# Performance work log

Hardware: AMD Instinct MI355X
Metric: run time of the kernel (lower is better)

## Reference

```python
import jax, jax.numpy as jnp
import numpy as np

B, S, D_MODEL = 1, 4096, 2048
N_HEADS, N_KV_HEADS, HEAD_DIM = 16, 4, 128
N_KV_GROUPS = N_HEADS // N_KV_HEADS  # 4


def rotate_half(x):
    h = x.shape[-1] // 2
    return jnp.concatenate([-x[..., h:], x[..., :h]], axis=-1)


def setup_inputs() -> dict:
    key = jax.random.key(0)
    k1, k2, k3, k4, k5 = jax.random.split(key, 5)
    hidden_states = jax.random.normal(k1, (B, S, D_MODEL), dtype=jnp.float32)
    # RoPE tables: [S, HEAD_DIM]
    inv_freq = 1.0 / (10000.0 ** (jnp.arange(0, HEAD_DIM, 2, dtype=jnp.float32) / HEAD_DIM))
    t = jnp.arange(S, dtype=jnp.float32)
    freqs = jnp.outer(t, inv_freq)                      # [S, HEAD_DIM/2]
    emb = jnp.concatenate([freqs, freqs], axis=-1)      # [S, HEAD_DIM]
    cos, sin = jnp.cos(emb), jnp.sin(emb)
    scale = 0.02
    Wq = jax.random.normal(k2, (D_MODEL, N_HEADS * HEAD_DIM), dtype=jnp.float32) * scale
    Wk = jax.random.normal(k3, (D_MODEL, N_KV_HEADS * HEAD_DIM), dtype=jnp.float32) * scale
    Wv = jax.random.normal(k4, (D_MODEL, N_KV_HEADS * HEAD_DIM), dtype=jnp.float32) * scale
    Wo = jax.random.normal(k5, (N_HEADS * HEAD_DIM, D_MODEL), dtype=jnp.float32) * scale
    return {"hidden_states": hidden_states, "cos": cos, "sin": sin,
            "Wq": Wq, "Wk": Wk, "Wv": Wv, "Wo": Wo}


def reference(hidden_states, cos, sin, Wq, Wk, Wv, Wo):
    b, s, _ = hidden_states.shape
    # projections -> [b, heads, s, head_dim]
    q = (hidden_states @ Wq).reshape(b, s, N_HEADS, HEAD_DIM).transpose(0, 2, 1, 3)
    k = (hidden_states @ Wk).reshape(b, s, N_KV_HEADS, HEAD_DIM).transpose(0, 2, 1, 3)
    v = (hidden_states @ Wv).reshape(b, s, N_KV_HEADS, HEAD_DIM).transpose(0, 2, 1, 3)
    # RoPE (cos/sin broadcast over batch and heads)
    c = cos[None, None, :, :]
    si = sin[None, None, :, :]
    q = q * c + rotate_half(q) * si
    k = k * c + rotate_half(k) * si
    # expand KV heads to match query heads (GQA)
    k = jnp.repeat(k, N_KV_GROUPS, axis=1)  # [b, N_HEADS, s, d]
    v = jnp.repeat(v, N_KV_GROUPS, axis=1)
    # attention scores with causal mask
    scores = jnp.einsum('bhqd,bhkd->bhqk', q, k) / jnp.sqrt(jnp.float32(HEAD_DIM))
    causal = jnp.tril(jnp.ones((s, s), dtype=bool))
    scores = jnp.where(causal[None, None], scores, jnp.float32(-jnp.inf))
    probs = jax.nn.softmax(scores.astype(jnp.float32), axis=-1).astype(q.dtype)
    out = jnp.einsum('bhqk,bhkd->bhqd', probs, v)
    out = out.transpose(0, 2, 1, 3).reshape(b, s, N_HEADS * HEAD_DIM)
    return out @ Wo
```

## Files before the change

### kernel.cpp

```cpp
#include <hip/hip_runtime.h>
#include <hip/hip_bf16.h>

#define S_LEN 4096
#define DMODEL 2048
#define NH 16
#define NKV 4
#define HD 128

typedef __bf16 bf16x8 __attribute__((ext_vector_type(8)));
typedef float f32x4 __attribute__((ext_vector_type(4)));
typedef unsigned short u16x8 __attribute__((ext_vector_type(8)));
typedef unsigned short u16x4 __attribute__((ext_vector_type(4)));
typedef unsigned long long u64x2 __attribute__((ext_vector_type(2)));

__device__ __forceinline__ unsigned short f2bf(float f) {
    unsigned int u = __builtin_bit_cast(unsigned int, f);
    u += 0x7fffu + ((u >> 16) & 1u);
    return (unsigned short)(u >> 16);
}
__device__ __forceinline__ float bf2f(unsigned short h) {
    unsigned int u = ((unsigned int)h) << 16;
    return __builtin_bit_cast(float, u);
}

__device__ __forceinline__ unsigned int cvt_pk_bf16(float lo, float hi) {
    unsigned int r;
    asm("v_cvt_pk_bf16_f32 %0, %1, %2" : "=v"(r) : "v"(lo), "v"(hi));
    return r;
}

__device__ __forceinline__ float fast_exp2(float x) {
    float r;
    asm("v_exp_f32 %0, %1" : "=v"(r) : "v"(x));
    return r;
}

__device__ __forceinline__ f32x4 mfma16(bf16x8 a, bf16x8 b, f32x4 c) {
    return __builtin_amdgcn_mfma_f32_16x16x32_bf16(a, b, c, 0, 0, 0);
}

__device__ __forceinline__ void async16(unsigned short* lds, const unsigned short* g) {
    __builtin_amdgcn_global_load_lds((__attribute__((address_space(1))) void*)g,
                                     (__attribute__((address_space(3))) void*)lds,
                                     16, 0, 0);
}

__global__ __launch_bounds__(256) void conv_f32_bf16(
    const float* __restrict__ in, unsigned short* __restrict__ out, int n4) {
    int i = blockIdx.x * 256 + threadIdx.x;
    if (i >= n4) return;
    float4 v = *(const float4*)&in[(size_t)i * 4];
    u16x4 o;
    o[0] = f2bf(v.x); o[1] = f2bf(v.y); o[2] = f2bf(v.z); o[3] = f2bf(v.w);
    *(u16x4*)&out[(size_t)i * 4] = o;
}

__global__ __launch_bounds__(1024) void transpose_f32_bf16(
    const float* __restrict__ in, unsigned short* __restrict__ out,
    int R, int C) {
    __shared__ float tile[32][33];
    int x = blockIdx.x * 32 + threadIdx.x;
    int y = blockIdx.y * 32 + threadIdx.y;
    tile[threadIdx.y][threadIdx.x] = in[(size_t)y * C + x];
    __syncthreads();
    int ox = blockIdx.y * 32 + threadIdx.x;
    int oy = blockIdx.x * 32 + threadIdx.y;
    out[(size_t)oy * R + ox] = f2bf(tile[threadIdx.x][threadIdx.y]);
}

__global__ __launch_bounds__(1024) void transpose_bf16(
    const unsigned short* __restrict__ in, unsigned short* __restrict__ out,
    int R, int C, int ldin) {
    __shared__ unsigned short tile[32][33];
    int x = blockIdx.x * 32 + threadIdx.x;
    int y = blockIdx.y * 32 + threadIdx.y;
    tile[threadIdx.y][threadIdx.x] = in[(size_t)y * ldin + x];
    __syncthreads();
    int ox = blockIdx.y * 32 + threadIdx.x;
    int oy = blockIdx.x * 32 + threadIdx.y;
    out[(size_t)oy * R + ox] = tile[threadIdx.x][threadIdx.y];
}

template <typename OutT>
__global__ __launch_bounds__(256) void gemm_bt(
    const unsigned short* __restrict__ A, const unsigned short* __restrict__ Bt,
    OutT* __restrict__ C, int N, int K) {
    __shared__ __align__(16) unsigned short As[2][128 * 32];
    __shared__ __align__(16) unsigned short Bs[2][128 * 32];
    const int tid = threadIdx.x;
    const int wave = tid >> 6, lane = tid & 63, quad = lane >> 4, l16 = lane & 15;
    const int m0 = blockIdx.x * 128, n0 = blockIdx.y * 128;
    const int waveM = (wave & 1) * 64, waveN = (wave >> 1) * 64;
    f32x4 acc[4][4] = {};

    auto stage = [&](int k0, int b) {
#pragma unroll
        for (int u = 0; u < 2; u++) {
            const int seg = wave * 2 + u;
            const int idx = seg * 64 + lane;
            const int r = idx >> 2, c = idx & 3;
            async16(&As[b][seg * 512], &A[(size_t)(m0 + r) * K + k0 + c * 8]);
            async16(&Bs[b][seg * 512], &Bt[(size_t)(n0 + r) * K + k0 + c * 8]);
        }
    };

    const int niter = K / 32;
    stage(0, 0);
    __syncthreads();
    for (int it = 0; it < niter; it++) {
        const int b = it & 1;
        if (it + 1 < niter) stage((it + 1) * 32, b ^ 1);
        bf16x8 af[4], bfv[4];
#pragma unroll
        for (int i = 0; i < 4; i++)
            af[i] = *(const bf16x8*)&As[b][(waveM + i * 16 + l16) * 32 + quad * 8];
#pragma unroll
        for (int j = 0; j < 4; j++)
            bfv[j] = *(const bf16x8*)&Bs[b][(waveN + j * 16 + l16) * 32 + quad * 8];
#pragma unroll
        for (int i = 0; i < 4; i++)
#pragma unroll
            for (int j = 0; j < 4; j++)
                acc[i][j] = mfma16(af[i], bfv[j], acc[i][j]);
        __syncthreads();
    }
#pragma unroll
    for (int i = 0; i < 4; i++)
#pragma unroll
        for (int j = 0; j < 4; j++)
#pragma unroll
            for (int r = 0; r < 4; r++) {
                int row = m0 + waveM + i * 16 + quad * 4 + r;
                int col = n0 + waveN + j * 16 + l16;
                if constexpr (sizeof(OutT) == 2)
                    C[(size_t)row * N + col] = f2bf(acc[i][j][r]);
                else
                    C[(size_t)row * N + col] = acc[i][j][r];
            }
}

__global__ __launch_bounds__(256) void rope_kernel(
    unsigned short* __restrict__ X, const float* __restrict__ cb,
    const float* __restrict__ sb, int log2nh, int stride) {
    int idx = blockIdx.x * 256 + threadIdx.x;
    int d = idx & 63;
    int h = (idx >> 6) & ((1 << log2nh) - 1);
    int s = idx >> (6 + log2nh);
    size_t base = (size_t)s * stride + h * HD + d;
    float a = bf2f(X[base]);
    float b = bf2f(X[base + 64]);
    float c0 = cb[s * HD + d];
    float s0 = sb[s * HD + d];
    float c1 = cb[s * HD + d + 64];
    float s1 = sb[s * HD + d + 64];
    X[base]      = f2bf(a * c0 - b * s0);
    X[base + 64] = f2bf(b * c1 + a * s1);
}

__global__ __launch_bounds__(256, 2) void attn_kernel(
    const unsigned short* __restrict__ Q, const unsigned short* __restrict__ Kv,
    const unsigned short* __restrict__ Vt, unsigned short* __restrict__ O) {
    __shared__ __align__(16) unsigned short Kt[2][64 * 128];
    __shared__ __align__(16) unsigned short Vs[2][128 * 64];
    __shared__ __align__(16) unsigned long long Ps[4 * 4 * 64];
    const int tid = threadIdx.x;
    const int wave = tid >> 6, lane = tid & 63, quad = lane >> 4, l16 = lane & 15;
    const int id = blockIdx.x;
    const int h = id & 15;
    const int qb = (id < 256) ? (31 - (id >> 4)) : ((id - 256) >> 4);
    const int kvh = h >> 2;
    const int rowbase = qb * 128 + wave * 32;
    unsigned long long* Pw = &Ps[wave * 4 * 64];
    const float cexp = 0.08838834764831845f * 1.44269504088896f;

    auto stage = [&](int c, int b) {
        const int kb = c * 64;
#pragma unroll
        for (int u = 0; u < 4; u++) {
            const int seg = wave * 4 + u;
            const int idx = seg * 64 + lane;
            {
                const int r = idx >> 4, cs = idx & 15, cl = cs ^ (r & 15);
                async16(&Kt[b][seg * 512],
                        &Kv[(size_t)(kb + r) * (NKV * HD * 2) + kvh * HD + cl * 8]);
            }
            {
                const int r = idx >> 3, cs = idx & 7, cl = cs ^ (r & 7);
                async16(&Vs[b][seg * 512],
                        &Vt[(size_t)(kvh * HD + r) * S_LEN + kb + cl * 8]);
            }
        }
    };

    bf16x8 qf[2][4];
#pragma unroll
    for (int i = 0; i < 2; i++)
#pragma unroll
        for (int dd = 0; dd < 4; dd++)
            qf[i][dd] = *(const bf16x8*)&Q[(size_t)(rowbase + i * 16 + l16) * DMODEL +
                                           h * HD + dd * 32 + quad * 8];

    f32x4 oacc[2][8] = {};
    float lrow[2] = {0.0f, 0.0f};
    const int qa0 = rowbase + l16;
    const int qa1 = rowbase + 16 + l16;
    const int nch = 2 * (qb + 1);

    stage(0, 0);
    __syncthreads();
    for (int c = 0; c < nch; c++) {
        const int b = c & 1;
        if (c + 1 < nch) stage(c + 1, b ^ 1);
        const int kb = c * 64;
        if (kb <= rowbase + 31) {
            const bool diag = (kb + 63 > rowbase);
#pragma unroll
            for (int kk = 0; kk < 2; kk++) {
                f32x4 sacc[2][2] = {};
                __builtin_amdgcn_s_setprio(1);
#pragma unroll
                for (int dd = 0; dd < 4; dd++) {
                    const int csw = (dd * 4 + quad) ^ l16;
                    bf16x8 kf0 = *(const bf16x8*)&Kt[b][(((2 * kk + 0) * 16 + l16) * 16 + csw) * 8];
                    bf16x8 kf1 = *(const bf16x8*)&Kt[b][(((2 * kk + 1) * 16 + l16) * 16 + csw) * 8];
                    sacc[0][0] = mfma16(kf0, qf[0][dd], sacc[0][0]);
                    sacc[0][1] = mfma16(kf1, qf[0][dd], sacc[0][1]);
                    sacc[1][0] = mfma16(kf0, qf[1][dd], sacc[1][0]);
                    sacc[1][1] = mfma16(kf1, qf[1][dd], sacc[1][1]);
                }
                __builtin_amdgcn_s_setprio(0);
#pragma unroll
                for (int i = 0; i < 2; i++) {
                    const int qa = i ? qa1 : qa0;
#pragma unroll
                    for (int jl = 0; jl < 2; jl++) {
                        const int kg = kb + 16 * (2 * kk + jl) + 4 * quad;
                        float p0 = fast_exp2(sacc[i][jl][0] * cexp);
                        float p1 = fast_exp2(sacc[i][jl][1] * cexp);
                        float p2 = fast_exp2(sacc[i][jl][2] * cexp);
                        float p3 = fast_exp2(sacc[i][jl][3] * cexp);
                        if (diag) {
                            if (kg + 0 > qa) p0 = 0.0f;
                            if (kg + 1 > qa) p1 = 0.0f;
                            if (kg + 2 > qa) p2 = 0.0f;
                            if (kg + 3 > qa) p3 = 0.0f;
                        }
                        lrow[i] += (p0 + p1) + (p2 + p3);
                        unsigned int lo = cvt_pk_bf16(p0, p1);
                        unsigned int hi = cvt_pk_bf16(p2, p3);
                        Pw[(i * 2 + jl) * 64 + lane] =
                            (unsigned long long)lo | ((unsigned long long)hi << 32);
                    }
                }
                bf16x8 pf[2];
#pragma unroll
                for (int i = 0; i < 2; i++) {
                    const unsigned long long* src =
                        &Pw[(i * 2 + (quad >> 1)) * 64 + l16 + 32 * (quad & 1)];
                    u64x2 t;
                    t[0] = src[0];
                    t[1] = src[16];
                    pf[i] = __builtin_bit_cast(bf16x8, t);
                }
                const int vsw0 = ((kk * 4 + quad) ^ (l16 & 7)) * 8;
                __builtin_amdgcn_s_setprio(1);
#pragma unroll
                for (int jd = 0; jd < 8; jd++) {
                    bf16x8 vf = *(const bf16x8*)&Vs[b][(jd * 16 + l16) * 64 + vsw0];
                    oacc[0][jd] = mfma16(pf[0], vf, oacc[0][jd]);
                    oacc[1][jd] = mfma16(pf[1], vf, oacc[1][jd]);
                }
                __builtin_amdgcn_s_setprio(0);
            }
        }
        __syncthreads();
    }
    float lsum[2];
#pragma unroll
    for (int i = 0; i < 2; i++) {
        float l = lrow[i];
        l += __shfl_xor(l, 16, 64);
        l += __shfl_xor(l, 32, 64);
        lsum[i] = l;
    }
#pragma unroll
    for (int i = 0; i < 2; i++)
#pragma unroll
        for (int r = 0; r < 4; r++) {
            float lq = __shfl(lsum[i], quad * 4 + r, 64);
            float inv = 1.0f / lq;
            int row = rowbase + i * 16 + quad * 4 + r;
#pragma unroll
            for (int jd = 0; jd < 8; jd++)
                O[(size_t)row * DMODEL + h * HD + jd * 16 + l16] = f2bf(oacc[i][jd][r] * inv);
        }
}

extern "C" void kernel_launch(void* const* d_in, const int* in_sizes, int n_in,
                              void* d_out, int out_size, void* d_ws, size_t ws_size,
                              hipStream_t stream) {
    const float* X  = (const float*)d_in[0];
    const float* cb = (const float*)d_in[1];
    const float* sb = (const float*)d_in[2];
    const float* Wq = (const float*)d_in[3];
    const float* Wk = (const float*)d_in[4];
    const float* Wv = (const float*)d_in[5];
    const float* Wo = (const float*)d_in[6];
    float* out = (float*)d_out;

    char* ws = (char*)d_ws;
    size_t off = 0;
    auto alloc = [&](size_t bytes) { char* p = ws + off; off += (bytes + 255) & ~(size_t)255; return p; };
    unsigned short* Xb   = (unsigned short*)alloc((size_t)S_LEN * DMODEL * 2);
    unsigned short* Qb   = (unsigned short*)alloc((size_t)S_LEN * DMODEL * 2);
    unsigned short* KVb  = (unsigned short*)alloc((size_t)S_LEN * 2 * NKV * HD * 2);
    unsigned short* Vtb  = (unsigned short*)alloc((size_t)S_LEN * NKV * HD * 2);
    unsigned short* Ob   = (unsigned short*)alloc((size_t)S_LEN * DMODEL * 2);
    unsigned short* WqT  = (unsigned short*)alloc((size_t)DMODEL * DMODEL * 2);
    unsigned short* WkvT = (unsigned short*)alloc((size_t)DMODEL * 2 * NKV * HD * 2);
    unsigned short* WoT  = (unsigned short*)alloc((size_t)DMODEL * DMODEL * 2);

    conv_f32_bf16<<<(S_LEN * DMODEL / 4 + 255) / 256, 256, 0, stream>>>(X, Xb, S_LEN * DMODEL / 4);

    dim3 tb(32, 32);
    transpose_f32_bf16<<<dim3(DMODEL / 32, DMODEL / 32), tb, 0, stream>>>(Wq, WqT, DMODEL, DMODEL);
    transpose_f32_bf16<<<dim3((NKV * HD) / 32, DMODEL / 32), tb, 0, stream>>>(Wk, WkvT, DMODEL, NKV * HD);
    transpose_f32_bf16<<<dim3((NKV * HD) / 32, DMODEL / 32), tb, 0, stream>>>(Wv, WkvT + (size_t)(NKV * HD) * DMODEL, DMODEL, NKV * HD);
    transpose_f32_bf16<<<dim3(DMODEL / 32, DMODEL / 32), tb, 0, stream>>>(Wo, WoT, DMODEL, DMODEL);

    gemm_bt<unsigned short><<<dim3(S_LEN / 128, DMODEL / 128), 256, 0, stream>>>(Xb, WqT, Qb, DMODEL, DMODEL);
    gemm_bt<unsigned short><<<dim3(S_LEN / 128, (2 * NKV * HD) / 128), 256, 0, stream>>>(Xb, WkvT, KVb, 2 * NKV * HD, DMODEL);

    rope_kernel<<<(S_LEN * NH * 64) / 256, 256, 0, stream>>>(Qb, cb, sb, 4, DMODEL);
    rope_kernel<<<(S_LEN * NKV * 64) / 256, 256, 0, stream>>>(KVb, cb, sb, 2, 2 * NKV * HD);

    transpose_bf16<<<dim3((NKV * HD) / 32, S_LEN / 32), tb, 0, stream>>>(
        KVb + NKV * HD, Vtb, S_LEN, NKV * HD, 2 * NKV * HD);

    attn_kernel<<<512, 256, 0, stream>>>(Qb, KVb, Vtb, Ob);

    gemm_bt<float><<<dim3(S_LEN / 128, DMODEL / 128), 256, 0, stream>>>(Ob, WoT, out, DMODEL, DMODEL);
}
```

Before: 420.4 us.

## Fuse QKV projection GEMM and halve attention tile to 64 query rows

Concatenates Wq, Wk and Wv into one transposed weight so a single GEMM produces Q, K and V in one interleaved buffer, replacing the two separate projection launches. The attention kernel is retiled from 128 query rows per block (32 per wave) to 64 (16 per wave), with 32-key chunks, smaller shared buffers, a new query-block ordering across 1024 blocks, and launch bounds raised to 4 blocks per CU. The smaller tiles aim for higher occupancy and better causal load balance, at the cost of less K/V reuse per load and more loop iterations and barriers.

After: 382.9 us. -8.9%, faster.

```diff
diff --git a/kernel.cpp b/kernel.cpp
--- a/kernel.cpp
+++ b/kernel.cpp
@@ -6,6 +6,7 @@
 #define NH 16
 #define NKV 4
 #define HD 128
+#define QKV_N 3072
 
 typedef __bf16 bf16x8 __attribute__((ext_vector_type(8)));
 typedef float f32x4 __attribute__((ext_vector_type(4)));
@@ -157,143 +158,128 @@
     X[base + 64] = f2bf(b * c1 + a * s1);
 }
 
-__global__ __launch_bounds__(256, 2) void attn_kernel(
+__global__ __launch_bounds__(256, 4) void attn_kernel(
     const unsigned short* __restrict__ Q, const unsigned short* __restrict__ Kv,
     const unsigned short* __restrict__ Vt, unsigned short* __restrict__ O) {
-    __shared__ __align__(16) unsigned short Kt[2][64 * 128];
-    __shared__ __align__(16) unsigned short Vs[2][128 * 64];
-    __shared__ __align__(16) unsigned long long Ps[4 * 4 * 64];
+    __shared__ __align__(16) unsigned short Kt[2][32 * 128];
+    __shared__ __align__(16) unsigned short Vs[2][128 * 32];
+    __shared__ __align__(16) unsigned long long Ps[4 * 2 * 64];
     const int tid = threadIdx.x;
     const int wave = tid >> 6, lane = tid & 63, quad = lane >> 4, l16 = lane & 15;
     const int id = blockIdx.x;
     const int h = id & 15;
-    const int qb = (id < 256) ? (31 - (id >> 4)) : ((id - 256) >> 4);
+    const int grp = id >> 4, g = grp & 15, quarter = grp >> 4;
+    const int qb = quarter == 0 ? 63 - g : quarter == 1 ? g
+                 : quarter == 2 ? 32 + g : 31 - g;
     const int kvh = h >> 2;
-    const int rowbase = qb * 128 + wave * 32;
-    unsigned long long* Pw = &Ps[wave * 4 * 64];
+    const int rowbase = qb * 64 + wave * 16;
+    unsigned long long* Pw = &Ps[wave * 2 * 64];
     const float cexp = 0.08838834764831845f * 1.44269504088896f;
 
     auto stage = [&](int c, int b) {
-        const int kb = c * 64;
-#pragma unroll
-        for (int u = 0; u < 4; u++) {
-            const int seg = wave * 4 + u;
+        const int kb = c * 32;
+#pragma unroll
+        for (int u = 0; u < 2; u++) {
+            const int seg = wave * 2 + u;
             const int idx = seg * 64 + lane;
             {
                 const int r = idx >> 4, cs = idx & 15, cl = cs ^ (r & 15);
                 async16(&Kt[b][seg * 512],
-                        &Kv[(size_t)(kb + r) * (NKV * HD * 2) + kvh * HD + cl * 8]);
+                        &Kv[(size_t)(kb + r) * QKV_N + kvh * HD + cl * 8]);
             }
             {
-                const int r = idx >> 3, cs = idx & 7, cl = cs ^ (r & 7);
+                const int r = idx >> 2, cs = idx & 3, cl = cs ^ ((r >> 1) & 3);
                 async16(&Vs[b][seg * 512],
                         &Vt[(size_t)(kvh * HD + r) * S_LEN + kb + cl * 8]);
             }
         }
     };
 
-    bf16x8 qf[2][4];
-#pragma unroll
-    for (int i = 0; i < 2; i++)
-#pragma unroll
-        for (int dd = 0; dd < 4; dd++)
-            qf[i][dd] = *(const bf16x8*)&Q[(size_t)(rowbase + i * 16 + l16) * DMODEL +
-                                           h * HD + dd * 32 + quad * 8];
-
-    f32x4 oacc[2][8] = {};
-    float lrow[2] = {0.0f, 0.0f};
-    const int qa0 = rowbase + l16;
-    const int qa1 = rowbase + 16 + l16;
-    const int nch = 2 * (qb + 1);
+    bf16x8 qf[4];
+#pragma unroll
+    for (int dd = 0; dd < 4; dd++)
+        qf[dd] = *(const bf16x8*)&Q[(size_t)(rowbase + l16) * QKV_N +
+                                     h * HD + dd * 32 + quad * 8];
+
+    f32x4 oacc[8] = {};
+    float lrow = 0.0f;
+    const int qa = rowbase + l16;
+    const int nch = 2 * qb + 2;
 
     stage(0, 0);
     __syncthreads();
     for (int c = 0; c < nch; c++) {
         const int b = c & 1;
         if (c + 1 < nch) stage(c + 1, b ^ 1);
-        const int kb = c * 64;
-        if (kb <= rowbase + 31) {
-            const bool diag = (kb + 63 > rowbase);
-#pragma unroll
-            for (int kk = 0; kk < 2; kk++) {
-                f32x4 sacc[2][2] = {};
-                __builtin_amdgcn_s_setprio(1);
-#pragma unroll
-                for (int dd = 0; dd < 4; dd++) {
-                    const int csw = (dd * 4 + quad) ^ l16;
-                    bf16x8 kf0 = *(const bf16x8*)&Kt[b][(((2 * kk + 0) * 16 + l16) * 16 + csw) * 8];
-                    bf16x8 kf1 = *(const bf16x8*)&Kt[b][(((2 * kk + 1) * 16 + l16) * 16 + csw) * 8];
-                    sacc[0][0] = mfma16(kf0, qf[0][dd], sacc[0][0]);
-                    sacc[0][1] = mfma16(kf1, qf[0][dd], sacc[0][1]);
-                    sacc[1][0] = mfma16(kf0, qf[1][dd], sacc[1][0]);
-                    sacc[1][1] = mfma16(kf1, qf[1][dd], sacc[1][1]);
+        const int kb = c * 32;
+        if (kb <= rowbase + 15) {
+            const bool diag = (kb + 31 > rowbase);
+            f32x4 sacc[2] = {};
+            __builtin_amdgcn_s_setprio(1);
+#pragma unroll
+            for (int dd = 0; dd < 4; dd++) {
+                const int csw = (dd * 4 + quad) ^ l16;
+                bf16x8 kf0 = *(const bf16x8*)&Kt[b][((0 * 16 + l16) * 16 + csw) * 8];
+                bf16x8 kf1 = *(const bf16x8*)&Kt[b][((1 * 16 + l16) * 16 + csw) * 8];
+                sacc[0] = mfma16(kf0, qf[dd], sacc[0]);
+                sacc[1] = mfma16(kf1, qf[dd], sacc[1]);
+            }
+            __builtin_amdgcn_s_setprio(0);
+#pragma unroll
+            for (int jl = 0; jl < 2; jl++) {
+                const int kg = kb + 16 * jl + 4 * quad;
+                float p0 = fast_exp2(sacc[jl][0] * cexp);
+                float p1 = fast_exp2(sacc[jl][1] * cexp);
+                float p2 = fast_exp2(sacc[jl][2] * cexp);
+                float p3 = fast_exp2(sacc[jl][3] * cexp);
+                if (diag) {
+                    if (kg + 0 > qa) p0 = 0.0f;
+                    if (kg + 1 > qa) p1 = 0.0f;
+                    if (kg + 2 > qa) p2 = 0.0f;
+                    if (kg + 3 > qa) p3 = 0.0f;
                 }
-                __builtin_amdgcn_s_setprio(0);
-#pragma unroll
-                for (int i = 0; i < 2; i++) {
-                    const int qa = i ? qa1 : qa0;
-#pragma unroll
-                    for (int jl = 0; jl < 2; jl++) {
-                        const int kg = kb + 16 * (2 * kk + jl) + 4 * quad;
-                        float p0 = fast_exp2(sacc[i][jl][0] * cexp);
-                        float p1 = fast_exp2(sacc[i][jl][1] * cexp);
-                        float p2 = fast_exp2(sacc[i][jl][2] * cexp);
-                        float p3 = fast_exp2(sacc[i][jl][3] * cexp);
-                        if (diag) {
-                            if (kg + 0 > qa) p0 = 0.0f;
-                            if (kg + 1 > qa) p1 = 0.0f;
-                            if (kg + 2 > qa) p2 = 0.0f;
-                            if (kg + 3 > qa) p3 = 0.0f;
-                        }
-                        lrow[i] += (p0 + p1) + (p2 + p3);
-                        unsigned int lo = cvt_pk_bf16(p0, p1);
-                        unsigned int hi = cvt_pk_bf16(p2, p3);
-                        Pw[(i * 2 + jl) * 64 + lane] =
-                            (unsigned long long)lo | ((unsigned long long)hi << 32);
-                    }
-                }
-                bf16x8 pf[2];
-#pragma unroll
-                for (int i = 0; i < 2; i++) {
-                    const unsigned long long* src =
-                        &Pw[(i * 2 + (quad >> 1)) * 64 + l16 + 32 * (quad & 1)];
-                    u64x2 t;
-                    t[0] = src[0];
-                    t[1] = src[16];
-                    pf[i] = __builtin_bit_cast(bf16x8, t);
-                }
-                const int vsw0 = ((kk * 4 + quad) ^ (l16 & 7)) * 8;
-                __builtin_amdgcn_s_setprio(1);
-#pragma unroll
-                for (int jd = 0; jd < 8; jd++) {
-                    bf16x8 vf = *(const bf16x8*)&Vs[b][(jd * 16 + l16) * 64 + vsw0];
-                    oacc[0][jd] = mfma16(pf[0], vf, oacc[0][jd]);
-                    oacc[1][jd] = mfma16(pf[1], vf, oacc[1][jd]);
-                }
-                __builtin_amdgcn_s_setprio(0);
-            }
+                lrow += (p0 + p1) + (p2 + p3);
+                unsigned int lo = cvt_pk_bf16(p0, p1);
+                unsigned int hi = cvt_pk_bf16(p2, p3);
+                Pw[jl * 64 + lane] =
+                    (unsigned long long)lo | ((unsigned long long)hi << 32);
+            }
+            bf16x8 pf;
+            {
+                const unsigned long long* src =
+                    &Pw[(quad >> 1) * 64 + l16 + 32 * (quad & 1)];
+                u64x2 t;
+                t[0] = src[0];
+                t[1] = src[16];
+                pf = __builtin_bit_cast(bf16x8, t);
+            }
+            const int vsw0 = (quad ^ ((l16 >> 1) & 3)) * 8;
+            __builtin_amdgcn_s_setprio(1);
+#pragma unroll
+            for (int jd = 0; jd < 8; jd++) {
+                bf16x8 vf = *(const bf16x8*)&Vs[b][(jd * 16 + l16) * 32 + vsw0];
+                oacc[jd] = mfma16(pf, vf, oacc[jd]);
+            }
+            __builtin_amdgcn_s_setprio(0);
         }
         __syncthreads();
     }
-    float lsum[2];
-#pragma unroll
-    for (int i = 0; i < 2; i++) {
-        float l = lrow[i];
+    float lsum;
+    {
+        float l = lrow;
         l += __shfl_xor(l, 16, 64);
         l += __shfl_xor(l, 32, 64);
-        lsum[i] = l;
+        lsum = l;
     }
 #pragma unroll
-    for (int i = 0; i < 2; i++)
-#pragma unroll
-        for (int r = 0; r < 4; r++) {
-            float lq = __shfl(lsum[i], quad * 4 + r, 64);
-            float inv = 1.0f / lq;
-            int row = rowbase + i * 16 + quad * 4 + r;
-#pragma unroll
-            for (int jd = 0; jd < 8; jd++)
-                O[(size_t)row * DMODEL + h * HD + jd * 16 + l16] = f2bf(oacc[i][jd][r] * inv);
-        }
+    for (int r = 0; r < 4; r++) {
+        float lq = __shfl(lsum, quad * 4 + r, 64);
+        float inv = 1.0f / lq;
+        int row = rowbase + quad * 4 + r;
+#pragma unroll
+        for (int jd = 0; jd < 8; jd++)
+            O[(size_t)row * DMODEL + h * HD + jd * 16 + l16] = f2bf(oacc[jd][r] * inv);
+    }
 }
 
 extern "C" void kernel_launch(void* const* d_in, const int* in_sizes, int n_in,
@@ -311,33 +297,30 @@
     char* ws = (char*)d_ws;
     size_t off = 0;
     auto alloc = [&](size_t bytes) { char* p = ws + off; off += (bytes + 255) & ~(size_t)255; return p; };
-    unsigned short* Xb   = (unsigned short*)alloc((size_t)S_LEN * DMODEL * 2);
-    unsigned short* Qb   = (unsigned short*)alloc((size_t)S_LEN * DMODEL * 2);
-    unsigned short* KVb  = (unsigned short*)alloc((size_t)S_LEN * 2 * NKV * HD * 2);
-    unsigned short* Vtb  = (unsigned short*)alloc((size_t)S_LEN * NKV * HD * 2);
-    unsigned short* Ob   = (unsigned short*)alloc((size_t)S_LEN * DMODEL * 2);
-    unsigned short* WqT  = (unsigned short*)alloc((size_t)DMODEL * DMODEL * 2);
-    unsigned short* WkvT = (unsigned short*)alloc((size_t)DMODEL * 2 * NKV * HD * 2);
-    unsigned short* WoT  = (unsigned short*)alloc((size_t)DMODEL * DMODEL * 2);
+    unsigned short* Xb    = (unsigned short*)alloc((size_t)S_LEN * DMODEL * 2);
+    unsigned short* QKVb  = (unsigned short*)alloc((size_t)S_LEN * QKV_N * 2);
+    unsigned short* Vtb   = (unsigned short*)alloc((size_t)S_LEN * NKV * HD * 2);
+    unsigned short* Ob    = (unsigned short*)alloc((size_t)S_LEN * DMODEL * 2);
+    unsigned short* WqkvT = (unsigned short*)alloc((size_t)QKV_N * DMODEL * 2);
+    unsigned short* WoT   = (unsigned short*)alloc((size_t)DMODEL * DMODEL * 2);
 
     conv_f32_bf16<<<(S_LEN * DMODEL / 4 + 255) / 256, 256, 0, stream>>>(X, Xb, S_LEN * DMODEL / 4);
 
     dim3 tb(32, 32);
-    transpose_f32_bf16<<<dim3(DMODEL / 32, DMODEL / 32), tb, 0, stream>>>(Wq, WqT, DMODEL, DMODEL);
-    transpose_f32_bf16<<<dim3((NKV * HD) / 32, DMODEL / 32), tb, 0, stream>>>(Wk, WkvT, DMODEL, NKV * HD);
-    transpose_f32_bf16<<<dim3((NKV * HD) / 32, DMODEL / 32), tb, 0, stream>>>(Wv, WkvT + (size_t)(NKV * HD) * DMODEL, DMODEL, NKV * HD);
+    transpose_f32_bf16<<<dim3(DMODEL / 32, DMODEL / 32), tb, 0, stream>>>(Wq, WqkvT, DMODEL, DMODEL);
+    transpose_f32_bf16<<<dim3((NKV * HD) / 32, DMODEL / 32), tb, 0, stream>>>(Wk, WqkvT + (size_t)DMODEL * DMODEL, DMODEL, NKV * HD);
+    transpose_f32_bf16<<<dim3((NKV * HD) / 32, DMODEL / 32), tb, 0, stream>>>(Wv, WqkvT + (size_t)(DMODEL + NKV * HD) * DMODEL, DMODEL, NKV * HD);
     transpose_f32_bf16<<<dim3(DMODEL / 32, DMODEL / 32), tb, 0, stream>>>(Wo, WoT, DMODEL, DMODEL);
 
-    gemm_bt<unsigned short><<<dim3(S_LEN / 128, DMODEL / 128), 256, 0, stream>>>(Xb, WqT, Qb, DMODEL, DMODEL);
-    gemm_bt<unsigned short><<<dim3(S_LEN / 128, (2 * NKV * HD) / 128), 256, 0, stream>>>(Xb, WkvT, KVb, 2 * NKV * HD, DMODEL);
-
-    rope_kernel<<<(S_LEN * NH * 64) / 256, 256, 0, stream>>>(Qb, cb, sb, 4, DMODEL);
-    rope_kernel<<<(S_LEN * NKV * 64) / 256, 256, 0, stream>>>(KVb, cb, sb, 2, 2 * NKV * HD);
+    gemm_bt<unsigned short><<<dim3(S_LEN / 128, QKV_N / 128), 256, 0, stream>>>(Xb, WqkvT, QKVb, QKV_N, DMODEL);
+
+    rope_kernel<<<(S_LEN * NH * 64) / 256, 256, 0, stream>>>(QKVb, cb, sb, 4, QKV_N);
+    rope_kernel<<<(S_LEN * NKV * 64) / 256, 256, 0, stream>>>(QKVb + DMODEL, cb, sb, 2, QKV_N);
 
     transpose_bf16<<<dim3((NKV * HD) / 32, S_LEN / 32), tb, 0, stream>>>(
-        KVb + NKV * HD, Vtb, S_LEN, NKV * HD, 2 * NKV * HD);
-
-    attn_kernel<<<512, 256, 0, stream>>>(Qb, KVb, Vtb, Ob);
+        QKVb + DMODEL + NKV * HD, Vtb, S_LEN, NKV * HD, QKV_N);
+
+    attn_kernel<<<1024, 256, 0, stream>>>(QKVb, QKVb + DMODEL, Vtb, Ob);
 
     gemm_bt<float><<<dim3(S_LEN / 128, DMODEL / 128), 256, 0, stream>>>(Ob, WoT, out, DMODEL, DMODEL);
 }
```

## Fuse Q and KV projections into one GEMM and halve attention KV tile

Applied to the files above, without the earlier changes.

The Q, K and V projections are merged into a single GEMM over a concatenated transposed weight, producing one interleaved QKV buffer. This removes a separate launch and fills the grid better. The attention kernel now stages 32-key chunks instead of 64, halving shared memory per block and raising the launch-bounds occupancy target from 2 to 4 blocks. The cost is twice as many barrier-synchronised iterations, each doing less MFMA work.

Measured after the change: 595.1 us. +41.6%, slower.

```diff
diff --git a/kernel.cpp b/kernel.cpp
--- a/kernel.cpp
+++ b/kernel.cpp
@@ -6,6 +6,7 @@
 #define NH 16
 #define NKV 4
 #define HD 128
+#define QKV_N 3072
 
 typedef __bf16 bf16x8 __attribute__((ext_vector_type(8)));
 typedef float f32x4 __attribute__((ext_vector_type(4)));
@@ -157,11 +158,11 @@
     X[base + 64] = f2bf(b * c1 + a * s1);
 }
 
-__global__ __launch_bounds__(256, 2) void attn_kernel(
+__global__ __launch_bounds__(256, 4) void attn_kernel(
     const unsigned short* __restrict__ Q, const unsigned short* __restrict__ Kv,
     const unsigned short* __restrict__ Vt, unsigned short* __restrict__ O) {
-    __shared__ __align__(16) unsigned short Kt[2][64 * 128];
-    __shared__ __align__(16) unsigned short Vs[2][128 * 64];
+    __shared__ __align__(16) unsigned short Kt[2][32 * 128];
+    __shared__ __align__(16) unsigned short Vs[2][128 * 32];
     __shared__ __align__(16) unsigned long long Ps[4 * 4 * 64];
     const int tid = threadIdx.x;
     const int wave = tid >> 6, lane = tid & 63, quad = lane >> 4, l16 = lane & 15;
@@ -174,18 +175,18 @@
     const float cexp = 0.08838834764831845f * 1.44269504088896f;
 
     auto stage = [&](int c, int b) {
-        const int kb = c * 64;
-#pragma unroll
-        for (int u = 0; u < 4; u++) {
-            const int seg = wave * 4 + u;
+        const int kb = c * 32;
+#pragma unroll
+        for (int u = 0; u < 2; u++) {
+            const int seg = wave * 2 + u;
             const int idx = seg * 64 + lane;
             {
                 const int r = idx >> 4, cs = idx & 15, cl = cs ^ (r & 15);
                 async16(&Kt[b][seg * 512],
-                        &Kv[(size_t)(kb + r) * (NKV * HD * 2) + kvh * HD + cl * 8]);
+                        &Kv[(size_t)(kb + r) * QKV_N + kvh * HD + cl * 8]);
             }
             {
-                const int r = idx >> 3, cs = idx & 7, cl = cs ^ (r & 7);
+                const int r = idx >> 2, cs = idx & 3, cl = cs ^ ((r >> 1) & 3);
                 async16(&Vs[b][seg * 512],
                         &Vt[(size_t)(kvh * HD + r) * S_LEN + kb + cl * 8]);
             }
@@ -197,81 +198,78 @@
     for (int i = 0; i < 2; i++)
 #pragma unroll
         for (int dd = 0; dd < 4; dd++)
-            qf[i][dd] = *(const bf16x8*)&Q[(size_t)(rowbase + i * 16 + l16) * DMODEL +
+            qf[i][dd] = *(const bf16x8*)&Q[(size_t)(rowbase + i * 16 + l16) * QKV_N +
                                            h * HD + dd * 32 + quad * 8];
 
     f32x4 oacc[2][8] = {};
     float lrow[2] = {0.0f, 0.0f};
     const int qa0 = rowbase + l16;
     const int qa1 = rowbase + 16 + l16;
-    const int nch = 2 * (qb + 1);
+    const int nch = 4 * qb + 4;
 
     stage(0, 0);
     __syncthreads();
     for (int c = 0; c < nch; c++) {
         const int b = c & 1;
         if (c + 1 < nch) stage(c + 1, b ^ 1);
-        const int kb = c * 64;
+        const int kb = c * 32;
         if (kb <= rowbase + 31) {
-            const bool diag = (kb + 63 > rowbase);
-#pragma unroll
-            for (int kk = 0; kk < 2; kk++) {
-                f32x4 sacc[2][2] = {};
-                __builtin_amdgcn_s_setprio(1);
-#pragma unroll
-                for (int dd = 0; dd < 4; dd++) {
-                    const int csw = (dd * 4 + quad) ^ l16;
-                    bf16x8 kf0 = *(const bf16x8*)&Kt[b][(((2 * kk + 0) * 16 + l16) * 16 + csw) * 8];
-                    bf16x8 kf1 = *(const bf16x8*)&Kt[b][(((2 * kk + 1) * 16 + l16) * 16 + csw) * 8];
-                    sacc[0][0] = mfma16(kf0, qf[0][dd], sacc[0][0]);
-                    sacc[0][1] = mfma16(kf1, qf[0][dd], sacc[0][1]);
-                    sacc[1][0] = mfma16(kf0, qf[1][dd], sacc[1][0]);
-                    sacc[1][1] = mfma16(kf1, qf[1][dd], sacc[1][1]);
+            const bool diag = (kb + 31 > rowbase);
+            f32x4 sacc[2][2] = {};
+            __builtin_amdgcn_s_setprio(1);
+#pragma unroll
+            for (int dd = 0; dd < 4; dd++) {
+                const int csw = (dd * 4 + quad) ^ l16;
+                bf16x8 kf0 = *(const bf16x8*)&Kt[b][((0 * 16 + l16) * 16 + csw) * 8];
+                bf16x8 kf1 = *(const bf16x8*)&Kt[b][((1 * 16 + l16) * 16 + csw) * 8];
+                sacc[0][0] = mfma16(kf0, qf[0][dd], sacc[0][0]);
+                sacc[0][1] = mfma16(kf1, qf[0][dd], sacc[0][1]);
+                sacc[1][0] = mfma16(kf0, qf[1][dd], sacc[1][0]);
+                sacc[1][1] = mfma16(kf1, qf[1][dd], sacc[1][1]);
+            }
+            __builtin_amdgcn_s_setprio(0);
+#pragma unroll
+            for (int i = 0; i < 2; i++) {
+                const int qa = i ? qa1 : qa0;
+#pragma unroll
+                for (int jl = 0; jl < 2; jl++) {
+                    const int kg = kb + 16 * jl + 4 * quad;
+                    float p0 = fast_exp2(sacc[i][jl][0] * cexp);
+                    float p1 = fast_exp2(sacc[i][jl][1] * cexp);
+                    float p2 = fast_exp2(sacc[i][jl][2] * cexp);
+                    float p3 = fast_exp2(sacc[i][jl][3] * cexp);
+                    if (diag) {
+                        if (kg + 0 > qa) p0 = 0.0f;
+                        if (kg + 1 > qa) p1 = 0.0f;
+                        if (kg + 2 > qa) p2 = 0.0f;
+                        if (kg + 3 > qa) p3 = 0.0f;
+                    }
+                    lrow[i] += (p0 + p1) + (p2 + p3);
+                    unsigned int lo = cvt_pk_bf16(p0, p1);
+                    unsigned int hi = cvt_pk_bf16(p2, p3);
+                    Pw[(i * 2 + jl) * 64 + lane] =
+                        (unsigned long long)lo | ((unsigned long long)hi << 32);
                 }
-                __builtin_amdgcn_s_setprio(0);
-#pragma unroll
-                for (int i = 0; i < 2; i++) {
-                    const int qa = i ? qa1 : qa0;
-#pragma unroll
-                    for (int jl = 0; jl < 2; jl++) {
-                        const int kg = kb + 16 * (2 * kk + jl) + 4 * quad;
-                        float p0 = fast_exp2(sacc[i][jl][0] * cexp);
-                        float p1 = fast_exp2(sacc[i][jl][1] * cexp);
-                        float p2 = fast_exp2(sacc[i][jl][2] * cexp);
-                        float p3 = fast_exp2(sacc[i][jl][3] * cexp);
-                        if (diag) {
-                            if (kg + 0 > qa) p0 = 0.0f;
-                            if (kg + 1 > qa) p1 = 0.0f;
-                            if (kg + 2 > qa) p2 = 0.0f;
-                            if (kg + 3 > qa) p3 = 0.0f;
-                        }
-                        lrow[i] += (p0 + p1) + (p2 + p3);
-                        unsigned int lo = cvt_pk_bf16(p0, p1);
-                        unsigned int hi = cvt_pk_bf16(p2, p3);
-                        Pw[(i * 2 + jl) * 64 + lane] =
-                            (unsigned long long)lo | ((unsigned long long)hi << 32);
-                    }
-                }
-                bf16x8 pf[2];
-#pragma unroll
-                for (int i = 0; i < 2; i++) {
-                    const unsigned long long* src =
-                        &Pw[(i * 2 + (quad >> 1)) * 64 + l16 + 32 * (quad & 1)];
-                    u64x2 t;
-                    t[0] = src[0];
-                    t[1] = src[16];
-                    pf[i] = __builtin_bit_cast(bf16x8, t);
-                }
-                const int vsw0 = ((kk * 4 + quad) ^ (l16 & 7)) * 8;
-                __builtin_amdgcn_s_setprio(1);
-#pragma unroll
-                for (int jd = 0; jd < 8; jd++) {
-                    bf16x8 vf = *(const bf16x8*)&Vs[b][(jd * 16 + l16) * 64 + vsw0];
-                    oacc[0][jd] = mfma16(pf[0], vf, oacc[0][jd]);
-                    oacc[1][jd] = mfma16(pf[1], vf, oacc[1][jd]);
-                }
-                __builtin_amdgcn_s_setprio(0);
-            }
+            }
+            bf16x8 pf[2];
+#pragma unroll
+            for (int i = 0; i < 2; i++) {
+                const unsigned long long* src =
+                    &Pw[(i * 2 + (quad >> 1)) * 64 + l16 + 32 * (quad & 1)];
+                u64x2 t;
+                t[0] = src[0];
+                t[1] = src[16];
+                pf[i] = __builtin_bit_cast(bf16x8, t);
+            }
+            const int vsw0 = (quad ^ ((l16 >> 1) & 3)) * 8;
+            __builtin_amdgcn_s_setprio(1);
+#pragma unroll
+            for (int jd = 0; jd < 8; jd++) {
+                bf16x8 vf = *(const bf16x8*)&Vs[b][(jd * 16 + l16) * 32 + vsw0];
+                oacc[0][jd] = mfma16(pf[0], vf, oacc[0][jd]);
+                oacc[1][jd] = mfma16(pf[1], vf, oacc[1][jd]);
+            }
+            __builtin_amdgcn_s_setprio(0);
         }
         __syncthreads();
     }
@@ -311,33 +309,30 @@
     char* ws = (char*)d_ws;
     size_t off = 0;
     auto alloc = [&](size_t bytes) { char* p = ws + off; off += (bytes + 255) & ~(size_t)255; return p; };
-    unsigned short* Xb   = (unsigned short*)alloc((size_t)S_LEN * DMODEL * 2);
-    unsigned short* Qb   = (unsigned short*)alloc((size_t)S_LEN * DMODEL * 2);
-    unsigned short* KVb  = (unsigned short*)alloc((size_t)S_LEN * 2 * NKV * HD * 2);
-    unsigned short* Vtb  = (unsigned short*)alloc((size_t)S_LEN * NKV * HD * 2);
-    unsigned short* Ob   = (unsigned short*)alloc((size_t)S_LEN * DMODEL * 2);
-    unsigned short* WqT  = (unsigned short*)alloc((size_t)DMODEL * DMODEL * 2);
-    unsigned short* WkvT = (unsigned short*)alloc((size_t)DMODEL * 2 * NKV * HD * 2);
-    unsigned short* WoT  = (unsigned short*)alloc((size_t)DMODEL * DMODEL * 2);
+    unsigned short* Xb    = (unsigned short*)alloc((size_t)S_LEN * DMODEL * 2);
+    unsigned short* QKVb  = (unsigned short*)alloc((size_t)S_LEN * QKV_N * 2);
+    unsigned short* Vtb   = (unsigned short*)alloc((size_t)S_LEN * NKV * HD * 2);
+    unsigned short* Ob    = (unsigned short*)alloc((size_t)S_LEN * DMODEL * 2);
+    unsigned short* WqkvT = (unsigned short*)alloc((size_t)QKV_N * DMODEL * 2);
+    unsigned short* WoT   = (unsigned short*)alloc((size_t)DMODEL * DMODEL * 2);
 
     conv_f32_bf16<<<(S_LEN * DMODEL / 4 + 255) / 256, 256, 0, stream>>>(X, Xb, S_LEN * DMODEL / 4);
 
     dim3 tb(32, 32);
-    transpose_f32_bf16<<<dim3(DMODEL / 32, DMODEL / 32), tb, 0, stream>>>(Wq, WqT, DMODEL, DMODEL);
-    transpose_f32_bf16<<<dim3((NKV * HD) / 32, DMODEL / 32), tb, 0, stream>>>(Wk, WkvT, DMODEL, NKV * HD);
-    transpose_f32_bf16<<<dim3((NKV * HD) / 32, DMODEL / 32), tb, 0, stream>>>(Wv, WkvT + (size_t)(NKV * HD) * DMODEL, DMODEL, NKV * HD);
+    transpose_f32_bf16<<<dim3(DMODEL / 32, DMODEL / 32), tb, 0, stream>>>(Wq, WqkvT, DMODEL, DMODEL);
+    transpose_f32_bf16<<<dim3((NKV * HD) / 32, DMODEL / 32), tb, 0, stream>>>(Wk, WqkvT + (size_t)DMODEL * DMODEL, DMODEL, NKV * HD);
+    transpose_f32_bf16<<<dim3((NKV * HD) / 32, DMODEL / 32), tb, 0, stream>>>(Wv, WqkvT + (size_t)(DMODEL + NKV * HD) * DMODEL, DMODEL, NKV * HD);
     transpose_f32_bf16<<<dim3(DMODEL / 32, DMODEL / 32), tb, 0, stream>>>(Wo, WoT, DMODEL, DMODEL);
 
-    gemm_bt<unsigned short><<<dim3(S_LEN / 128, DMODEL / 128), 256, 0, stream>>>(Xb, WqT, Qb, DMODEL, DMODEL);
-    gemm_bt<unsigned short><<<dim3(S_LEN / 128, (2 * NKV * HD) / 128), 256, 0, stream>>>(Xb, WkvT, KVb, 2 * NKV * HD, DMODEL);
-
-    rope_kernel<<<(S_LEN * NH * 64) / 256, 256, 0, stream>>>(Qb, cb, sb, 4, DMODEL);
-    rope_kernel<<<(S_LEN * NKV * 64) / 256, 256, 0, stream>>>(KVb, cb, sb, 2, 2 * NKV * HD);
+    gemm_bt<unsigned short><<<dim3(S_LEN / 128, QKV_N / 128), 256, 0, stream>>>(Xb, WqkvT, QKVb, QKV_N, DMODEL);
+
+    rope_kernel<<<(S_LEN * NH * 64) / 256, 256, 0, stream>>>(QKVb, cb, sb, 4, QKV_N);
+    rope_kernel<<<(S_LEN * NKV * 64) / 256, 256, 0, stream>>>(QKVb + DMODEL, cb, sb, 2, QKV_N);
 
     transpose_bf16<<<dim3((NKV * HD) / 32, S_LEN / 32), tb, 0, stream>>>(
-        KVb + NKV * HD, Vtb, S_LEN, NKV * HD, 2 * NKV * HD);
-
-    attn_kernel<<<512, 256, 0, stream>>>(Qb, KVb, Vtb, Ob);
+        QKVb + DMODEL + NKV * HD, Vtb, S_LEN, NKV * HD, QKV_N);
+
+    attn_kernel<<<512, 256, 0, stream>>>(QKVb, QKVb + DMODEL, Vtb, Ob);
 
     gemm_bt<float><<<dim3(S_LEN / 128, DMODEL / 128), 256, 0, stream>>>(Ob, WoT, out, DMODEL, DMODEL);
 }
```
